# Optimization experiments

Measured on AMD Instinct MI355X. Metric: run time of the kernel, lower is better.

## Reference

```python
import jax, jax.numpy as jnp
import numpy as np

ENT_SIZE = 250000
REL_SIZE = 64
EMBED = 128
B = 32768
K = 8


def setup_inputs() -> dict:
    key = jax.random.key(0)
    ks = jax.random.split(key, 9)
    initrange = 0.5 / EMBED
    u = lambda k, n: jax.random.uniform(k, (n, EMBED), jnp.float32, -initrange, initrange)
    V = ENT_SIZE + REL_SIZE  # unified vocab: entities first, then relations
    return {
        "in_ent_w": u(ks[0], ENT_SIZE),
        "out_ent_w": u(ks[1], ENT_SIZE),
        "in_rel_w": u(ks[2], REL_SIZE),
        "out_rel_w": u(ks[3], REL_SIZE),
        "in_map_w": u(ks[4], REL_SIZE),
        "out_map_w": u(ks[5], REL_SIZE),
        "input_labels": jax.random.randint(ks[6], (B,), 0, V, jnp.int32),
        "pos_labels": jax.random.randint(ks[7], (B,), 0, V, jnp.int32),
        "neg_labels": jax.random.randint(ks[8], (B, K), 0, V, jnp.int32),
    }


def _map(ent, mapping):
    # project ent onto the hyperplane normal to normalize(mapping)  (TransH-style)
    n = mapping / jnp.maximum(jnp.linalg.norm(mapping, axis=-1, keepdims=True), 1e-12)
    return ent - jnp.sum(ent * n, axis=-1, keepdims=True) * n


def _pair_embs(iid, pid, is_ent_i, is_ent_p, in_ent_w, out_ent_w, in_rel_w, out_rel_w, in_map_w, out_map_w):
    """Per-row (input_emb, output_emb) per the 4 mask branches, plus the stable
    permutation that reproduces torch's boolean-mask + concat row ordering."""
    rel_size = in_rel_w.shape[0]
    iid_r = jnp.minimum(iid, rel_size - 1)  # clip: only used where label is a relation
    pid_r = jnp.minimum(pid, rel_size - 1)
    e_in = in_ent_w[iid]        # [N, D]
    r_in = in_rel_w[iid_r]
    e_out = out_ent_w[pid]
    r_out = out_rel_w[pid_r]
    mp_in = in_map_w[pid_r]
    mp_out = out_map_w[iid_r]
    mi = is_ent_i[:, None]
    mp = is_ent_p[:, None]
    inp = jnp.where(mi, jnp.where(mp, e_in, _map(e_in, mp_in)), r_in)
    out = jnp.where(mp, jnp.where(mi, e_out, _map(e_out, mp_out)), r_out)
    # branch key: 0=(ent,ent) 1=(ent,rel) 2=(rel,ent) 3=(rel,rel) -> concat order
    branch = (~is_ent_i).astype(jnp.int32) * 2 + (~is_ent_p).astype(jnp.int32)
    perm = jnp.argsort(branch, stable=True)
    return inp[perm], out[perm]


def reference(in_ent_w, out_ent_w, in_rel_w, out_rel_w, in_map_w, out_map_w,
              input_labels, pos_labels, neg_labels):
    ent_size = in_ent_w.shape[0]
    b, k = neg_labels.shape
    neg_flat = neg_labels.reshape(-1)

    # reverse_id_map: entity labels keep id, relation labels offset by ent_size
    to_id = lambda lab: jnp.where(lab < ent_size, lab, lab - ent_size)
    is_ent = lambda lab: lab < ent_size

    iid, pid, nid = to_id(input_labels), to_id(pos_labels), to_id(neg_flat)
    ii, ip, inn = is_ent(input_labels), is_ent(pos_labels), is_ent(neg_flat)

    Ws = (in_ent_w, out_ent_w, in_rel_w, out_rel_w, in_map_w, out_map_w)

    inp_pos, out_pos = _pair_embs(iid, pid, ii, ip, *Ws)
    iid_rep = jnp.repeat(iid, k)
    ii_rep = jnp.repeat(ii, k)
    inp_neg, out_neg = _pair_embs(iid_rep, nid, ii_rep, inn, *Ws)

    log_pos = jax.nn.log_sigmoid(jnp.sum(out_pos * inp_pos, axis=-1))          # [B]
    log_neg = jax.nn.log_sigmoid(jnp.sum(out_neg * (-inp_neg), axis=-1))       # [B*K]
    log_neg = log_neg.reshape(b, k).sum(axis=1)                                # [B]
    return -(log_pos + log_neg)
```

## Files before the change

kernel.cpp:

```cpp
#include <hip/hip_runtime.h>
#include <hip/hip_bf16.h>
#include <stdint.h>

#define ENT 250000
#define RELSZ 64
#define D 128
#define BATCH 32768
#define KNEG 8


__device__ __forceinline__ float block128_reduce(float v, float* lds, int t) {
#pragma unroll
  for (int off = 32; off > 0; off >>= 1) v += __shfl_down(v, off, 64);
  __syncthreads();
  if ((t & 63) == 0) lds[t >> 6] = v;
  __syncthreads();
  return lds[0] + lds[1];
}

__device__ __forceinline__ float logsig(float x) {
  return fminf(x, 0.f) - log1pf(expf(-fabsf(x)));
}

__global__ void k_tables(const float* __restrict__ in_rel, const float* __restrict__ out_rel,
                         const float* __restrict__ in_map, const float* __restrict__ out_map,
                         float* __restrict__ t1, float* __restrict__ t2, float* __restrict__ RR) {
  int p = blockIdx.x, t = threadIdx.x;
  __shared__ float lds[2];
  __shared__ float sri[128];
  float im = in_map[p * D + t], om = out_map[p * D + t];
  float ro = out_rel[p * D + t], ri = in_rel[p * D + t];
  float s_im2 = block128_reduce(im * im, lds, t);
  float n_im = im / fmaxf(sqrtf(s_im2), 1e-12f);
  float s_om2 = block128_reduce(om * om, lds, t);
  float n_om = om / fmaxf(sqrtf(s_om2), 1e-12f);
  float d1 = block128_reduce(n_im * ro, lds, t);
  float d2 = block128_reduce(n_om * ri, lds, t);
  t1[p * D + t] = ro - d1 * n_im;
  t2[p * D + t] = ri - d2 * n_om;
  sri[t] = ri;
  __syncthreads();
  if (t < RELSZ) {
    const float* rq = out_rel + t * D;
    float s = 0.f;
#pragma unroll 8
    for (int d = 0; d < D; d += 4) {
      float4 r4 = *(const float4*)(rq + d);
      s += sri[d] * r4.x + sri[d + 1] * r4.y + sri[d + 2] * r4.z + sri[d + 3] * r4.w;
    }
    RR[p * RELSZ + t] = s;
  }
}

__global__ void k_count(const int* __restrict__ in_lab, const int* __restrict__ pos_lab,
                        const int* __restrict__ neg_lab, uint8_t* __restrict__ keys,
                        int* __restrict__ C) {
  int blk = blockIdx.x, t = threadIdx.x;
  int wave = t >> 6, lane = t & 63;
  int key;
  if (blk < 128) {
    int i = blk * 256 + t;
    int il = in_lab[i], pl = pos_lab[i];
    key = ((il >= ENT) ? 2 : 0) | ((pl >= ENT) ? 1 : 0);
    keys[i] = (uint8_t)key;
  } else {
    int i = (blk - 128) * 256 + t;
    int il = in_lab[i >> 3], nl = neg_lab[i];
    key = ((il >= ENT) ? 2 : 0) | ((nl >= ENT) ? 1 : 0);
    keys[BATCH + i] = (uint8_t)key;
  }
  __shared__ int wc[4][4];
  unsigned long long m[4];
#pragma unroll
  for (int v = 0; v < 4; v++) m[v] = __ballot(key == v);
  if (lane < 4) wc[wave][lane] = __popcll(m[lane]);
  __syncthreads();
  if (t < 4) {
    int s = wc[0][t] + wc[1][t] + wc[2][t] + wc[3][t];
    int idx = (blk < 128) ? (t * 128 + blk) : (512 + t * 1024 + (blk - 128));
    C[idx] = s;
  }
}

__global__ void k_scan(int* __restrict__ C) {
  int t = threadIdx.x, lane = t & 63, w = t >> 6;
  int base = t * 18;
  int v[18];
  int s = 0;
#pragma unroll
  for (int j = 0; j < 18; j++) { v[j] = C[base + j]; s += v[j]; }
  int inc = s;
#pragma unroll
  for (int off = 1; off < 64; off <<= 1) {
    int x = __shfl_up(inc, off, 64);
    if (lane >= off) inc += x;
  }
  __shared__ int wsum[4];
  if (lane == 63) wsum[w] = inc;
  __syncthreads();
  int wpre = 0;
  for (int i = 0; i < w; i++) wpre += wsum[i];
  int run = wpre + inc - s;
#pragma unroll
  for (int j = 0; j < 18; j++) { C[base + j] = run; run += v[j]; }
}

__global__ void k_dest(const uint8_t* __restrict__ keys, const int* __restrict__ C,
                       int* __restrict__ dest_pos, int* __restrict__ dest_neg) {
  int blk = blockIdx.x, t = threadIdx.x;
  int wave = t >> 6, lane = t & 63;
  bool is_pos = blk < 128;
  int i, key;
  if (is_pos) { i = blk * 256 + t; key = keys[i]; }
  else        { i = (blk - 128) * 256 + t; key = keys[BATCH + i]; }
  __shared__ int wc[4][4];
  unsigned long long m[4];
#pragma unroll
  for (int v = 0; v < 4; v++) m[v] = __ballot(key == v);
  if (lane < 4) wc[wave][lane] = __popcll(m[lane]);
  int wrank = __popcll(m[key] & ((1ull << lane) - 1ull));
  __syncthreads();
  int wpre = 0;
  for (int w = 0; w < wave; w++) wpre += wc[w][key];
  int idx = is_pos ? (key * 128 + blk) : (512 + key * 1024 + (blk - 128));
  int dest = C[idx] + wpre + wrank;
  if (is_pos) dest_pos[i] = dest;
  else        dest_neg[i] = dest - BATCH;
}

__global__ void k_main(const float* __restrict__ in_ent, const float* __restrict__ out_ent,
                       const float* __restrict__ t1, const float* __restrict__ t2,
                       const float* __restrict__ RR,
                       const int* __restrict__ in_lab, const int* __restrict__ pos_lab,
                       const int* __restrict__ neg_lab,
                       const int* __restrict__ dest_pos, const int* __restrict__ dest_neg,
                       float* __restrict__ buf_pos, float* __restrict__ buf_neg) {
  int b = (blockIdx.x * blockDim.x + threadIdx.x) >> 6;
  int lane = threadIdx.x & 63;
  int q = lane & 15, g = lane >> 4;

  int il = in_lab[b];
  bool ei = il < ENT;
  int iid = ei ? il : il - ENT;
  const float* Lp = ei ? (in_ent + (size_t)iid * D) : (t2 + (size_t)iid * D);
  float4 La = *(const float4*)(Lp + q * 8);
  float4 Lb = *(const float4*)(Lp + q * 8 + 4);

  int ol0 = pos_lab[b];
  int ol1 = neg_lab[b * 8 + 0], ol2 = neg_lab[b * 8 + 1], ol3 = neg_lab[b * 8 + 2];
  int ol4 = neg_lab[b * 8 + 3], ol5 = neg_lab[b * 8 + 4], ol6 = neg_lab[b * 8 + 5];
  int ol7 = neg_lab[b * 8 + 6], ol8 = neg_lab[b * 8 + 7];

  int oA = (g == 0) ? ol0 : (g == 1) ? ol1 : (g == 2) ? ol2 : ol3;
  int oB = (g == 0) ? ol4 : (g == 1) ? ol5 : (g == 2) ? ol6 : ol7;
  int oC = ol8;

  float4 RaA, RbA, RaB, RbB, RaC, RbC;
  {
    bool e = oA < ENT; int oid = e ? oA : oA - ENT;
    const float* Rp = (e ? out_ent : t1) + (size_t)oid * D + q * 8;
    RaA = *(const float4*)(Rp); RbA = *(const float4*)(Rp + 4);
  }
  {
    bool e = oB < ENT; int oid = e ? oB : oB - ENT;
    const float* Rp = (e ? out_ent : t1) + (size_t)oid * D + q * 8;
    RaB = *(const float4*)(Rp); RbB = *(const float4*)(Rp + 4);
  }
  {
    bool e = oC < ENT; int oid = e ? oC : oC - ENT;
    const float* Rp = (e ? out_ent : t1) + (size_t)oid * D + q * 8;
    RaC = *(const float4*)(Rp); RbC = *(const float4*)(Rp + 4);
  }

  float pA = La.x * RaA.x + La.y * RaA.y + La.z * RaA.z + La.w * RaA.w +
             Lb.x * RbA.x + Lb.y * RbA.y + Lb.z * RbA.z + Lb.w * RbA.w;
  float pB = La.x * RaB.x + La.y * RaB.y + La.z * RaB.z + La.w * RaB.w +
             Lb.x * RbB.x + Lb.y * RbB.y + Lb.z * RbB.z + Lb.w * RbB.w;
  float pC = La.x * RaC.x + La.y * RaC.y + La.z * RaC.z + La.w * RaC.w +
             Lb.x * RbC.x + Lb.y * RbC.y + Lb.z * RbC.z + Lb.w * RbC.w;
#pragma unroll
  for (int off = 8; off > 0; off >>= 1) {
    pA += __shfl_xor(pA, off, 64);
    pB += __shfl_xor(pB, off, 64);
    pC += __shfl_xor(pC, off, 64);
  }
  if (!ei) {
    if (oA >= ENT) pA = RR[iid * RELSZ + (oA - ENT)];
    if (oB >= ENT) pB = RR[iid * RELSZ + (oB - ENT)];
    if (oC >= ENT) pC = RR[iid * RELSZ + (oC - ENT)];
  }

  if (q == 0) {
    if (g == 0) buf_pos[dest_pos[b]] = logsig(pA);
    else        buf_neg[dest_neg[b * 8 + g - 1]] = logsig(-pA);
    buf_neg[dest_neg[b * 8 + g + 3]] = logsig(-pB);
    if (g == 0) buf_neg[dest_neg[b * 8 + 7]] = logsig(-pC);
  }
}

__global__ void k_combine(const float* __restrict__ buf_pos, const float* __restrict__ buf_neg,
                          float* __restrict__ out) {
  int j = blockIdx.x * blockDim.x + threadIdx.x;
  if (j >= BATCH) return;
  float4 a = ((const float4*)buf_neg)[j * 2];
  float4 b = ((const float4*)buf_neg)[j * 2 + 1];
  float s = a.x + a.y + a.z + a.w + b.x + b.y + b.z + b.w;
  out[j] = -(buf_pos[j] + s);
}

extern "C" void kernel_launch(void* const* d_in, const int* in_sizes, int n_in,
                              void* d_out, int out_size, void* d_ws, size_t ws_size,
                              hipStream_t stream) {
  const float* in_ent  = (const float*)d_in[0];
  const float* out_ent = (const float*)d_in[1];
  const float* in_rel  = (const float*)d_in[2];
  const float* out_rel = (const float*)d_in[3];
  const float* in_map  = (const float*)d_in[4];
  const float* out_map = (const float*)d_in[5];
  const int* in_lab  = (const int*)d_in[6];
  const int* pos_lab = (const int*)d_in[7];
  const int* neg_lab = (const int*)d_in[8];

  char* ws = (char*)d_ws;
  float*   t1       = (float*)(ws + 0);
  float*   t2       = (float*)(ws + 32768);
  float*   RR       = (float*)(ws + 65536);
  int*     C        = (int*)(ws + 81920);
  uint8_t* keys     = (uint8_t*)(ws + 102400);
  int*     dest_pos = (int*)(ws + 397312);
  int*     dest_neg = (int*)(ws + 528384);
  float*   buf_pos  = (float*)(ws + 1576960);
  float*   buf_neg  = (float*)(ws + 1708032);
  float*   out      = (float*)d_out;

  k_tables<<<64, 128, 0, stream>>>(in_rel, out_rel, in_map, out_map, t1, t2, RR);
  k_count<<<1152, 256, 0, stream>>>(in_lab, pos_lab, neg_lab, keys, C);
  k_scan<<<1, 256, 0, stream>>>(C);
  k_dest<<<1152, 256, 0, stream>>>(keys, C, dest_pos, dest_neg);
  k_main<<<8192, 256, 0, stream>>>(in_ent, out_ent, t1, t2, RR,
                                   in_lab, pos_lab, neg_lab, dest_pos, dest_neg,
                                   buf_pos, buf_neg);
  k_combine<<<128, 256, 0, stream>>>(buf_pos, buf_neg, out);
}
```

Baseline: 53.93 us.

## Merge prep kernels, compute destinations in main kernel, accumulate output with atomics

Fuses the relation-table kernel and the count kernel into a single prep kernel that also stores per-element ranks as 16-bit values and zeroes the output. The separate destination and combine kernels are removed. The main kernel computes destinations from the scanned counts plus ranks and atomically adds the log-sigmoid terms into the output. It also remaps lanes so each group of 8 lanes handles one of 8 output rows plus a shared ninth. This cuts kernel launches and intermediate buffer traffic, at the cost of atomic contention and nondeterministic summation order.

```diff
diff --git a/kernel.cpp b/kernel.cpp
--- a/kernel.cpp
+++ b/kernel.cpp
@@ -9,77 +9,106 @@
 #define KNEG 8
 
 
-__device__ __forceinline__ float block128_reduce(float v, float* lds, int t) {
-#pragma unroll
-  for (int off = 32; off > 0; off >>= 1) v += __shfl_down(v, off, 64);
-  __syncthreads();
-  if ((t & 63) == 0) lds[t >> 6] = v;
-  __syncthreads();
-  return lds[0] + lds[1];
-}
-
 __device__ __forceinline__ float logsig(float x) {
   return fminf(x, 0.f) - log1pf(expf(-fabsf(x)));
 }
 
-__global__ void k_tables(const float* __restrict__ in_rel, const float* __restrict__ out_rel,
-                         const float* __restrict__ in_map, const float* __restrict__ out_map,
-                         float* __restrict__ t1, float* __restrict__ t2, float* __restrict__ RR) {
-  int p = blockIdx.x, t = threadIdx.x;
-  __shared__ float lds[2];
-  __shared__ float sri[128];
-  float im = in_map[p * D + t], om = out_map[p * D + t];
-  float ro = out_rel[p * D + t], ri = in_rel[p * D + t];
-  float s_im2 = block128_reduce(im * im, lds, t);
-  float n_im = im / fmaxf(sqrtf(s_im2), 1e-12f);
-  float s_om2 = block128_reduce(om * om, lds, t);
-  float n_om = om / fmaxf(sqrtf(s_om2), 1e-12f);
-  float d1 = block128_reduce(n_im * ro, lds, t);
-  float d2 = block128_reduce(n_om * ri, lds, t);
-  t1[p * D + t] = ro - d1 * n_im;
-  t2[p * D + t] = ri - d2 * n_om;
-  sri[t] = ri;
-  __syncthreads();
-  if (t < RELSZ) {
-    const float* rq = out_rel + t * D;
-    float s = 0.f;
+__global__ void k_prep(const float* __restrict__ in_rel, const float* __restrict__ out_rel,
+                       const float* __restrict__ in_map, const float* __restrict__ out_map,
+                       const int* __restrict__ in_lab, const int* __restrict__ pos_lab,
+                       const int* __restrict__ neg_lab,
+                       float* __restrict__ t1, float* __restrict__ t2, float* __restrict__ RR,
+                       int* __restrict__ C, uint16_t* __restrict__ rank_pos,
+                       uint16_t* __restrict__ rank_neg, float* __restrict__ out) {
+  __shared__ float ls[4];
+  __shared__ float sri[2][128];
+  __shared__ int wc[4][4];
+  int blk = blockIdx.x, t = threadIdx.x;
+
+  if (blk >= 1152) {
+    int sub = t >> 7, tt = t & 127;
+    int p = (blk - 1152) * 2 + sub;
+    float im = in_map[p * D + tt], om = out_map[p * D + tt];
+    float ro = out_rel[p * D + tt], ri = in_rel[p * D + tt];
+    float v, r;
+    float n_im, n_om;
+    v = im * im;
+#pragma unroll
+    for (int off = 32; off > 0; off >>= 1) v += __shfl_xor(v, off, 64);
+    if ((t & 63) == 0) ls[t >> 6] = v;
+    __syncthreads();
+    r = ls[sub * 2] + ls[sub * 2 + 1];
+    n_im = im / fmaxf(sqrtf(r), 1e-12f);
+    __syncthreads();
+    v = om * om;
+#pragma unroll
+    for (int off = 32; off > 0; off >>= 1) v += __shfl_xor(v, off, 64);
+    if ((t & 63) == 0) ls[t >> 6] = v;
+    __syncthreads();
+    r = ls[sub * 2] + ls[sub * 2 + 1];
+    n_om = om / fmaxf(sqrtf(r), 1e-12f);
+    __syncthreads();
+    v = n_im * ro;
+#pragma unroll
+    for (int off = 32; off > 0; off >>= 1) v += __shfl_xor(v, off, 64);
+    if ((t & 63) == 0) ls[t >> 6] = v;
+    __syncthreads();
+    float d1 = ls[sub * 2] + ls[sub * 2 + 1];
+    __syncthreads();
+    v = n_om * ri;
+#pragma unroll
+    for (int off = 32; off > 0; off >>= 1) v += __shfl_xor(v, off, 64);
+    if ((t & 63) == 0) ls[t >> 6] = v;
+    __syncthreads();
+    float d2 = ls[sub * 2] + ls[sub * 2 + 1];
+    t1[p * D + tt] = ro - d1 * n_im;
+    t2[p * D + tt] = ri - d2 * n_om;
+    sri[sub][tt] = ri;
+    __syncthreads();
+    int half = t >> 7, lq = t & 127;
+    if (lq < RELSZ) {
+      int pr = (blk - 1152) * 2 + half;
+      const float* rq = out_rel + lq * D;
+      const float* s = sri[half];
+      float acc = 0.f;
 #pragma unroll 8
-    for (int d = 0; d < D; d += 4) {
-      float4 r4 = *(const float4*)(rq + d);
-      s += sri[d] * r4.x + sri[d + 1] * r4.y + sri[d + 2] * r4.z + sri[d + 3] * r4.w;
-    }
-    RR[p * RELSZ + t] = s;
-  }
-}
-
-__global__ void k_count(const int* __restrict__ in_lab, const int* __restrict__ pos_lab,
-                        const int* __restrict__ neg_lab, uint8_t* __restrict__ keys,
-                        int* __restrict__ C) {
-  int blk = blockIdx.x, t = threadIdx.x;
+      for (int d = 0; d < D; d += 4) {
+        float4 r4 = *(const float4*)(rq + d);
+        acc += s[d] * r4.x + s[d + 1] * r4.y + s[d + 2] * r4.z + s[d + 3] * r4.w;
+      }
+      RR[pr * RELSZ + lq] = acc;
+    }
+    return;
+  }
+
   int wave = t >> 6, lane = t & 63;
-  int key;
-  if (blk < 128) {
-    int i = blk * 256 + t;
+  int key, i;
+  bool is_pos = blk < 128;
+  if (is_pos) {
+    i = blk * 256 + t;
     int il = in_lab[i], pl = pos_lab[i];
     key = ((il >= ENT) ? 2 : 0) | ((pl >= ENT) ? 1 : 0);
-    keys[i] = (uint8_t)key;
   } else {
-    int i = (blk - 128) * 256 + t;
+    i = (blk - 128) * 256 + t;
     int il = in_lab[i >> 3], nl = neg_lab[i];
     key = ((il >= ENT) ? 2 : 0) | ((nl >= ENT) ? 1 : 0);
-    keys[BATCH + i] = (uint8_t)key;
-  }
-  __shared__ int wc[4][4];
+  }
   unsigned long long m[4];
 #pragma unroll
   for (int v = 0; v < 4; v++) m[v] = __ballot(key == v);
   if (lane < 4) wc[wave][lane] = __popcll(m[lane]);
+  int wrank = __popcll(m[key] & ((1ull << lane) - 1ull));
   __syncthreads();
   if (t < 4) {
     int s = wc[0][t] + wc[1][t] + wc[2][t] + wc[3][t];
-    int idx = (blk < 128) ? (t * 128 + blk) : (512 + t * 1024 + (blk - 128));
+    int idx = is_pos ? (t * 128 + blk) : (512 + t * 1024 + (blk - 128));
     C[idx] = s;
   }
+  int wpre = 0;
+  for (int w = 0; w < wave; w++) wpre += wc[w][key];
+  uint16_t rk = (uint16_t)(wpre + wrank);
+  if (is_pos) { rank_pos[i] = rk; out[i] = 0.f; }
+  else        { rank_neg[i] = rk; }
 }
 
 __global__ void k_scan(int* __restrict__ C) {
@@ -105,107 +134,84 @@
   for (int j = 0; j < 18; j++) { C[base + j] = run; run += v[j]; }
 }
 
-__global__ void k_dest(const uint8_t* __restrict__ keys, const int* __restrict__ C,
-                       int* __restrict__ dest_pos, int* __restrict__ dest_neg) {
-  int blk = blockIdx.x, t = threadIdx.x;
-  int wave = t >> 6, lane = t & 63;
-  bool is_pos = blk < 128;
-  int i, key;
-  if (is_pos) { i = blk * 256 + t; key = keys[i]; }
-  else        { i = (blk - 128) * 256 + t; key = keys[BATCH + i]; }
-  __shared__ int wc[4][4];
-  unsigned long long m[4];
-#pragma unroll
-  for (int v = 0; v < 4; v++) m[v] = __ballot(key == v);
-  if (lane < 4) wc[wave][lane] = __popcll(m[lane]);
-  int wrank = __popcll(m[key] & ((1ull << lane) - 1ull));
-  __syncthreads();
-  int wpre = 0;
-  for (int w = 0; w < wave; w++) wpre += wc[w][key];
-  int idx = is_pos ? (key * 128 + blk) : (512 + key * 1024 + (blk - 128));
-  int dest = C[idx] + wpre + wrank;
-  if (is_pos) dest_pos[i] = dest;
-  else        dest_neg[i] = dest - BATCH;
-}
-
 __global__ void k_main(const float* __restrict__ in_ent, const float* __restrict__ out_ent,
                        const float* __restrict__ t1, const float* __restrict__ t2,
                        const float* __restrict__ RR,
                        const int* __restrict__ in_lab, const int* __restrict__ pos_lab,
                        const int* __restrict__ neg_lab,
-                       const int* __restrict__ dest_pos, const int* __restrict__ dest_neg,
-                       float* __restrict__ buf_pos, float* __restrict__ buf_neg) {
-  int b = (blockIdx.x * blockDim.x + threadIdx.x) >> 6;
+                       const int* __restrict__ C, const uint16_t* __restrict__ rank_pos,
+                       const uint16_t* __restrict__ rank_neg, float* __restrict__ out) {
+  int b = __builtin_amdgcn_readfirstlane((int)((blockIdx.x * blockDim.x + threadIdx.x) >> 6));
   int lane = threadIdx.x & 63;
-  int q = lane & 15, g = lane >> 4;
+  int q = lane & 7, g = lane >> 3;
 
   int il = in_lab[b];
   bool ei = il < ENT;
   int iid = ei ? il : il - ENT;
-  const float* Lp = ei ? (in_ent + (size_t)iid * D) : (t2 + (size_t)iid * D);
-  float4 La = *(const float4*)(Lp + q * 8);
-  float4 Lb = *(const float4*)(Lp + q * 8 + 4);
-
-  int ol0 = pos_lab[b];
-  int ol1 = neg_lab[b * 8 + 0], ol2 = neg_lab[b * 8 + 1], ol3 = neg_lab[b * 8 + 2];
-  int ol4 = neg_lab[b * 8 + 3], ol5 = neg_lab[b * 8 + 4], ol6 = neg_lab[b * 8 + 5];
-  int ol7 = neg_lab[b * 8 + 6], ol8 = neg_lab[b * 8 + 7];
-
-  int oA = (g == 0) ? ol0 : (g == 1) ? ol1 : (g == 2) ? ol2 : ol3;
-  int oB = (g == 0) ? ol4 : (g == 1) ? ol5 : (g == 2) ? ol6 : ol7;
-  int oC = ol8;
-
-  float4 RaA, RbA, RaB, RbB, RaC, RbC;
-  {
-    bool e = oA < ENT; int oid = e ? oA : oA - ENT;
-    const float* Rp = (e ? out_ent : t1) + (size_t)oid * D + q * 8;
-    RaA = *(const float4*)(Rp); RbA = *(const float4*)(Rp + 4);
-  }
-  {
-    bool e = oB < ENT; int oid = e ? oB : oB - ENT;
-    const float* Rp = (e ? out_ent : t1) + (size_t)oid * D + q * 8;
-    RaB = *(const float4*)(Rp); RbB = *(const float4*)(Rp + 4);
-  }
-  {
-    bool e = oC < ENT; int oid = e ? oC : oC - ENT;
-    const float* Rp = (e ? out_ent : t1) + (size_t)oid * D + q * 8;
-    RaC = *(const float4*)(Rp); RbC = *(const float4*)(Rp + 4);
-  }
-
-  float pA = La.x * RaA.x + La.y * RaA.y + La.z * RaA.z + La.w * RaA.w +
-             Lb.x * RbA.x + Lb.y * RbA.y + Lb.z * RbA.z + Lb.w * RbA.w;
-  float pB = La.x * RaB.x + La.y * RaB.y + La.z * RaB.z + La.w * RaB.w +
-             Lb.x * RbB.x + Lb.y * RbB.y + Lb.z * RbB.z + Lb.w * RbB.w;
-  float pC = La.x * RaC.x + La.y * RaC.y + La.z * RaC.z + La.w * RaC.w +
-             Lb.x * RbC.x + Lb.y * RbC.y + Lb.z * RbC.z + Lb.w * RbC.w;
-#pragma unroll
-  for (int off = 8; off > 0; off >>= 1) {
+  const float* Lp = (ei ? in_ent + (size_t)iid * D : t2 + (size_t)iid * D) + q * 4;
+  float4 L0 = *(const float4*)(Lp);
+  float4 L1 = *(const float4*)(Lp + 32);
+  float4 L2 = *(const float4*)(Lp + 64);
+  float4 L3 = *(const float4*)(Lp + 96);
+
+  int oA = (g == 0) ? pos_lab[b] : neg_lab[b * 8 + g - 1];
+  int oB = neg_lab[b * 8 + 7];
+  int keyA = (ei ? 0 : 2) | ((oA < ENT) ? 0 : 1);
+  int keyB = (ei ? 0 : 2) | ((oB < ENT) ? 0 : 1);
+
+  int dA = 0, dB = 0;
+  if (q == 0) {
+    if (g == 0) {
+      dA = C[keyA * 128 + (b >> 8)] + (int)rank_pos[b];
+    } else {
+      int i = b * 8 + g - 1;
+      dA = (C[512 + keyA * 1024 + (i >> 8)] + (int)rank_neg[i] - BATCH) >> 3;
+    }
+    if (g == 7) {
+      int i = b * 8 + 7;
+      dB = (C[512 + keyB * 1024 + (i >> 8)] + (int)rank_neg[i] - BATCH) >> 3;
+    }
+  }
+
+  bool eA = oA < ENT; int oidA = eA ? oA : oA - ENT;
+  const float* RpA = (eA ? out_ent + (size_t)oidA * D : t1 + (size_t)oidA * D) + q * 4;
+  float4 A0 = *(const float4*)(RpA);
+  float4 A1 = *(const float4*)(RpA + 32);
+  float4 A2 = *(const float4*)(RpA + 64);
+  float4 A3 = *(const float4*)(RpA + 96);
+
+  bool eB = oB < ENT; int oidB = eB ? oB : oB - ENT;
+  const float* RpB = (eB ? out_ent + (size_t)oidB * D : t1 + (size_t)oidB * D) + q * 4;
+  float4 B0 = *(const float4*)(RpB);
+  float4 B1 = *(const float4*)(RpB + 32);
+  float4 B2 = *(const float4*)(RpB + 64);
+  float4 B3 = *(const float4*)(RpB + 96);
+
+  float pA = L0.x * A0.x + L0.y * A0.y + L0.z * A0.z + L0.w * A0.w +
+             L1.x * A1.x + L1.y * A1.y + L1.z * A1.z + L1.w * A1.w +
+             L2.x * A2.x + L2.y * A2.y + L2.z * A2.z + L2.w * A2.w +
+             L3.x * A3.x + L3.y * A3.y + L3.z * A3.z + L3.w * A3.w;
+  float pB = L0.x * B0.x + L0.y * B0.y + L0.z * B0.z + L0.w * B0.w +
+             L1.x * B1.x + L1.y * B1.y + L1.z * B1.z + L1.w * B1.w +
+             L2.x * B2.x + L2.y * B2.y + L2.z * B2.z + L2.w * B2.w +
+             L3.x * B3.x + L3.y * B3.y + L3.z * B3.z + L3.w * B3.w;
+#pragma unroll
+  for (int off = 4; off > 0; off >>= 1) {
     pA += __shfl_xor(pA, off, 64);
     pB += __shfl_xor(pB, off, 64);
-    pC += __shfl_xor(pC, off, 64);
-  }
-  if (!ei) {
-    if (oA >= ENT) pA = RR[iid * RELSZ + (oA - ENT)];
-    if (oB >= ENT) pB = RR[iid * RELSZ + (oB - ENT)];
-    if (oC >= ENT) pC = RR[iid * RELSZ + (oC - ENT)];
   }
 
   if (q == 0) {
-    if (g == 0) buf_pos[dest_pos[b]] = logsig(pA);
-    else        buf_neg[dest_neg[b * 8 + g - 1]] = logsig(-pA);
-    buf_neg[dest_neg[b * 8 + g + 3]] = logsig(-pB);
-    if (g == 0) buf_neg[dest_neg[b * 8 + 7]] = logsig(-pC);
-  }
-}
-
-__global__ void k_combine(const float* __restrict__ buf_pos, const float* __restrict__ buf_neg,
-                          float* __restrict__ out) {
-  int j = blockIdx.x * blockDim.x + threadIdx.x;
-  if (j >= BATCH) return;
-  float4 a = ((const float4*)buf_neg)[j * 2];
-  float4 b = ((const float4*)buf_neg)[j * 2 + 1];
-  float s = a.x + a.y + a.z + a.w + b.x + b.y + b.z + b.w;
-  out[j] = -(buf_pos[j] + s);
+    float dotA = pA;
+    if (!ei && oA >= ENT) dotA = RR[iid * RELSZ + (oA - ENT)];
+    float vA = (g == 0) ? logsig(dotA) : logsig(-dotA);
+    atomicAdd(out + dA, -vA);
+    if (g == 7) {
+      float dotB = pB;
+      if (!ei && oB >= ENT) dotB = RR[iid * RELSZ + (oB - ENT)];
+      atomicAdd(out + dB, -logsig(-dotB));
+    }
+  }
 }
 
 extern "C" void kernel_launch(void* const* d_in, const int* in_sizes, int n_in,
@@ -222,23 +228,19 @@
   const int* neg_lab = (const int*)d_in[8];
 
   char* ws = (char*)d_ws;
-  float*   t1       = (float*)(ws + 0);
-  float*   t2       = (float*)(ws + 32768);
-  float*   RR       = (float*)(ws + 65536);
-  int*     C        = (int*)(ws + 81920);
-  uint8_t* keys     = (uint8_t*)(ws + 102400);
-  int*     dest_pos = (int*)(ws + 397312);
-  int*     dest_neg = (int*)(ws + 528384);
-  float*   buf_pos  = (float*)(ws + 1576960);
-  float*   buf_neg  = (float*)(ws + 1708032);
-  float*   out      = (float*)d_out;
-
-  k_tables<<<64, 128, 0, stream>>>(in_rel, out_rel, in_map, out_map, t1, t2, RR);
-  k_count<<<1152, 256, 0, stream>>>(in_lab, pos_lab, neg_lab, keys, C);
+  float*    t1       = (float*)(ws + 0);
+  float*    t2       = (float*)(ws + 32768);
+  float*    RR       = (float*)(ws + 65536);
+  int*      C        = (int*)(ws + 81920);
+  uint16_t* rank_pos = (uint16_t*)(ws + 100352);
+  uint16_t* rank_neg = (uint16_t*)(ws + 165888);
+  float*    out      = (float*)d_out;
+
+  k_prep<<<1184, 256, 0, stream>>>(in_rel, out_rel, in_map, out_map,
+                                   in_lab, pos_lab, neg_lab,
+                                   t1, t2, RR, C, rank_pos, rank_neg, out);
   k_scan<<<1, 256, 0, stream>>>(C);
-  k_dest<<<1152, 256, 0, stream>>>(keys, C, dest_pos, dest_neg);
   k_main<<<8192, 256, 0, stream>>>(in_ent, out_ent, t1, t2, RR,
-                                   in_lab, pos_lab, neg_lab, dest_pos, dest_neg,
-                                   buf_pos, buf_neg);
-  k_combine<<<128, 256, 0, stream>>>(buf_pos, buf_neg, out);
-}
+                                   in_lab, pos_lab, neg_lab,
+                                   C, rank_pos, rank_neg, out);
+}
```

New measurement: 46.74 us. 1.15x faster.
